# Kernel tuning notes

Measured on AMD Instinct MI355X. Metric: run time of the kernel, lower is better.

The kernel has to match this reference:

```python
import jax, jax.numpy as jnp
import numpy as np

K_BITS = 8
D_V = 32

# 256-entry popcount lookup table (float, matching torch buffer)
_POP_LUT = jnp.asarray(np.array([bin(i).count('1') for i in range(256)], dtype=np.float32))


def setup_inputs() -> dict:
    key = jax.random.key(0)
    k1, k2, k3 = jax.random.split(key, 3)
    B, H, W = 8, 64, 64
    z = jax.random.uniform(k1, (B, K_BITS, H, W), dtype=jnp.float32)
    temperature = jnp.asarray(1.0, dtype=jnp.float32)
    value_embed = jax.random.normal(k2, (256, D_V), dtype=jnp.float32)  # nn.Embedding default N(0,1)
    return {"z": z, "temperature": temperature, "value_embed": value_embed}


def reference(z, temperature, value_embed):
    B, k, H, W = z.shape
    N = H * W
    d_v = value_embed.shape[1]
    # bitpack: threshold to {0,1}, pack k bits into one byte code per position
    bits = (z > 0.5).astype(jnp.int32)                       # (B,k,H,W)
    shifts = (2 ** jnp.arange(k, dtype=jnp.int32)).reshape(1, k, 1, 1)
    codes = (bits * shifts).sum(axis=1).reshape(B, N)        # (B,N) in [0,255]
    # pairwise Hamming distance via XOR + LUT popcount
    xor = codes[:, :, None] ^ codes[:, None, :]              # (B,N,N) int
    dist = _POP_LUT[xor]                                     # (B,N,N) float
    scores = -dist / jnp.clip(temperature, 0.1)
    attn = jax.nn.softmax(scores, axis=-1)                   # (B,N,N)
    values = value_embed[jnp.clip(codes, 0, 255)]            # (B,N,d_v)
    ctx = jnp.einsum('bnm,bmd->bnd', attn, values)           # (B,N,d_v)
    return ctx.transpose(0, 2, 1).reshape(B, d_v, H, W)
```

## Files before the change

kernel.cpp:

```cpp
#include <hip/hip_runtime.h>
#include <hip/hip_bf16.h>

#define B_SZ   8
#define KBITS  8
#define NPOS   4096
#define DV     32
#define NCODE  256
#define NSLICE 32

__global__ __launch_bounds__(1024) void k_fused(const float* __restrict__ z,
                                                const float* __restrict__ V,
                                                const float* __restrict__ temp,
                                                float* __restrict__ out) {
    const int b   = blockIdx.x >> 5;
    const int s   = blockIdx.x & (NSLICE - 1);
    const int tid = threadIdx.x;

    __shared__ unsigned int codes_u[NPOS / 4];
    __shared__ int h[NCODE];
    __shared__ float T[NCODE * (DV + 1)];

    if (tid < NCODE) h[tid] = 0;
    __syncthreads();

    {
        const float4* z4 = (const float4*)(z + (size_t)b * KBITS * NPOS);
        unsigned int c0 = 0, c1 = 0, c2 = 0, c3 = 0;
#pragma unroll
        for (int bit = 0; bit < KBITS; ++bit) {
            const float4 f = z4[bit * (NPOS / 4) + tid];
            c0 |= (unsigned)(f.x > 0.5f) << bit;
            c1 |= (unsigned)(f.y > 0.5f) << bit;
            c2 |= (unsigned)(f.z > 0.5f) << bit;
            c3 |= (unsigned)(f.w > 0.5f) << bit;
        }
        codes_u[tid] = c0 | (c1 << 8) | (c2 << 16) | (c3 << 24);
        atomicAdd(&h[c0], 1);
        atomicAdd(&h[c1], 1);
        atomicAdd(&h[c2], 1);
        atomicAdd(&h[c3], 1);
    }
    __syncthreads();

    const int d = tid >> 5;
    const int l = tid & 31;
    const float a = __expf(-1.0f / fmaxf(temp[0], 0.1f));

    float val[8], cnt[8];
#pragma unroll
    for (int j = 0; j < 8; ++j) {
        const int v = l * 8 + j;
        const float c = (float)h[v];
        cnt[j] = c;
        val[j] = c * V[v * DV + d];
    }

#pragma unroll
    for (int st = 0; st < 3; ++st) {
        const int m = 1 << st;
#pragma unroll
        for (int j = 0; j < 8; ++j) {
            if ((j & m) == 0) {
                const int j1 = j | m;
                const float v0 = val[j], v1 = val[j1];
                val[j]  = fmaf(a, v1, v0);
                val[j1] = fmaf(a, v0, v1);
                const float s0 = cnt[j], s1 = cnt[j1];
                cnt[j]  = fmaf(a, s1, s0);
                cnt[j1] = fmaf(a, s0, s1);
            }
        }
    }
#pragma unroll
    for (int st = 0; st < 5; ++st) {
        const int m = 1 << st;
#pragma unroll
        for (int j = 0; j < 8; ++j) {
            const float pv = __shfl_xor(val[j], m);
            val[j] = fmaf(a, pv, val[j]);
            const float pc = __shfl_xor(cnt[j], m);
            cnt[j] = fmaf(a, pc, cnt[j]);
        }
    }

#pragma unroll
    for (int j = 0; j < 8; ++j) {
        const int c = l * 8 + j;
        T[c * (DV + 1) + d] = val[j] / cnt[j];
    }
    __syncthreads();

    {
        const unsigned char* cb = (const unsigned char*)codes_u;
        const int ng   = tid & 31;
        const int base = s * 128 + ng * 4;
        const uchar4 cc = *(const uchar4*)(cb + base);
        float4 r;
        r.x = T[cc.x * (DV + 1) + d];
        r.y = T[cc.y * (DV + 1) + d];
        r.z = T[cc.z * (DV + 1) + d];
        r.w = T[cc.w * (DV + 1) + d];
        float4* o4 = (float4*)(out + (size_t)(b * DV + d) * NPOS + base);
        *o4 = r;
    }
}

extern "C" void kernel_launch(void* const* d_in, const int* in_sizes, int n_in,
                              void* d_out, int out_size, void* d_ws, size_t ws_size,
                              hipStream_t stream) {
    const float* z    = (const float*)d_in[0];
    const float* temp = (const float*)d_in[1];
    const float* V    = (const float*)d_in[2];
    float* out        = (float*)d_out;

    k_fused<<<B_SZ * NSLICE, 1024, 0, stream>>>(z, V, temp, out);
}
```

Measured before the change: 66.86 us.

## Split code packing and histogram into a separate pass to avoid redundant recompute

Before, each of the 32 slice blocks per batch re-read all of z for its batch and rebuilt the full code array and histogram, which is 32x redundant global traffic. A first kernel now packs codes and per-slice partial histograms into workspace, and the second kernel sums 32 partials per bin, builds the table and gathers its output slice. This removes the redundant z reads but adds a second launch and a round trip through global memory.

```diff
diff --git a/kernel.cpp b/kernel.cpp
--- a/kernel.cpp
+++ b/kernel.cpp
@@ -1,5 +1,4 @@
 #include <hip/hip_runtime.h>
-#include <hip/hip_bf16.h>
 
 #define B_SZ   8
 #define KBITS  8
@@ -8,7 +7,45 @@
 #define NCODE  256
 #define NSLICE 32
 
-__global__ __launch_bounds__(1024) void k_fused(const float* __restrict__ z,
+
+__global__ __launch_bounds__(256) void k_codes(const float* __restrict__ z,
+                                               unsigned int* __restrict__ codes_g,
+                                               int* __restrict__ partial_g) {
+    const int blk = blockIdx.x;
+    const int b   = blk >> 5;
+    const int s   = blk & (NSLICE - 1);
+    const int t   = threadIdx.x;
+
+    __shared__ int h[NCODE];
+    h[t] = 0;
+    __syncthreads();
+
+    const int j   = t >> 3;
+    const int bit = t & 7;
+    const float4 f = ((const float4*)z)[b * (KBITS * NPOS / 4) +
+                                        bit * (NPOS / 4) + s * 32 + j];
+    unsigned int p = ((unsigned)(f.x > 0.5f) << bit)
+                   | ((unsigned)(f.y > 0.5f) << (8  + bit))
+                   | ((unsigned)(f.z > 0.5f) << (16 + bit))
+                   | ((unsigned)(f.w > 0.5f) << (24 + bit));
+    p |= __shfl_xor(p, 1);
+    p |= __shfl_xor(p, 2);
+    p |= __shfl_xor(p, 4);
+
+    if (bit == 0) {
+        codes_g[b * (NPOS / 4) + s * 32 + j] = p;
+        atomicAdd(&h[p & 255], 1);
+        atomicAdd(&h[(p >> 8) & 255], 1);
+        atomicAdd(&h[(p >> 16) & 255], 1);
+        atomicAdd(&h[p >> 24], 1);
+    }
+    __syncthreads();
+
+    partial_g[blk * NCODE + t] = h[t];
+}
+
+__global__ __launch_bounds__(1024) void k_table(const unsigned int* __restrict__ codes_g,
+                                                const int* __restrict__ partial_g,
                                                 const float* __restrict__ V,
                                                 const float* __restrict__ temp,
                                                 float* __restrict__ out) {
@@ -16,29 +53,20 @@
     const int s   = blockIdx.x & (NSLICE - 1);
     const int tid = threadIdx.x;
 
-    __shared__ unsigned int codes_u[NPOS / 4];
-    __shared__ int h[NCODE];
+    __shared__ int   h[NCODE];
     __shared__ float T[NCODE * (DV + 1)];
 
     if (tid < NCODE) h[tid] = 0;
     __syncthreads();
 
     {
-        const float4* z4 = (const float4*)(z + (size_t)b * KBITS * NPOS);
-        unsigned int c0 = 0, c1 = 0, c2 = 0, c3 = 0;
+        const int bin = tid & 255;
+        const int q   = tid >> 8;
+        const int* pg = partial_g + (b * NSLICE + q * 8) * NCODE + bin;
+        int sum = 0;
 #pragma unroll
-        for (int bit = 0; bit < KBITS; ++bit) {
-            const float4 f = z4[bit * (NPOS / 4) + tid];
-            c0 |= (unsigned)(f.x > 0.5f) << bit;
-            c1 |= (unsigned)(f.y > 0.5f) << bit;
-            c2 |= (unsigned)(f.z > 0.5f) << bit;
-            c3 |= (unsigned)(f.w > 0.5f) << bit;
-        }
-        codes_u[tid] = c0 | (c1 << 8) | (c2 << 16) | (c3 << 24);
-        atomicAdd(&h[c0], 1);
-        atomicAdd(&h[c1], 1);
-        atomicAdd(&h[c2], 1);
-        atomicAdd(&h[c3], 1);
+        for (int i = 0; i < 8; ++i) sum += pg[i * NCODE];
+        atomicAdd(&h[bin], sum);
     }
     __syncthreads();
 
@@ -91,15 +119,14 @@
     __syncthreads();
 
     {
-        const unsigned char* cb = (const unsigned char*)codes_u;
         const int ng   = tid & 31;
         const int base = s * 128 + ng * 4;
-        const uchar4 cc = *(const uchar4*)(cb + base);
+        const unsigned int cw = codes_g[b * (NPOS / 4) + s * 32 + ng];
         float4 r;
-        r.x = T[cc.x * (DV + 1) + d];
-        r.y = T[cc.y * (DV + 1) + d];
-        r.z = T[cc.z * (DV + 1) + d];
-        r.w = T[cc.w * (DV + 1) + d];
+        r.x = T[(cw         & 255) * (DV + 1) + d];
+        r.y = T[((cw >> 8)  & 255) * (DV + 1) + d];
+        r.z = T[((cw >> 16) & 255) * (DV + 1) + d];
+        r.w = T[(cw >> 24)         * (DV + 1) + d];
         float4* o4 = (float4*)(out + (size_t)(b * DV + d) * NPOS + base);
         *o4 = r;
     }
@@ -113,5 +140,9 @@
     const float* V    = (const float*)d_in[2];
     float* out        = (float*)d_out;
 
-    k_fused<<<B_SZ * NSLICE, 1024, 0, stream>>>(z, V, temp, out);
+    unsigned int* codes_g = (unsigned int*)d_ws;
+    int* partial_g        = (int*)d_ws + B_SZ * (NPOS / 4);
+
+    k_codes<<<B_SZ * NSLICE, 256, 0, stream>>>(z, codes_g, partial_g);
+    k_table<<<B_SZ * NSLICE, 1024, 0, stream>>>(codes_g, partial_g, V, temp, out);
 }
```

Measured after the change: 66.32 us. No clear change (-0.8%).
